# Kernel optimization log

Measured on AMD Instinct MI355X. Metric: run time of the kernel, lower is better.

Reference implementation:

```python
import jax, jax.numpy as jnp
import numpy as np

B, K, D, DK, DG, H = 4, 512, 768, 96, 96, 8  # batch, proposals, appearance, key, geo, n_relations


def setup_inputs() -> dict:
    key = jax.random.key(0)
    ks = jax.random.split(key, 12)
    s = 0.02
    return {
        "f_a": jax.random.normal(ks[0], (B, K, D), dtype=jnp.float32),
        "position_embedding": jax.random.uniform(ks[1], (B, K, K, DG), dtype=jnp.float32),
        "WG_w": jax.random.normal(ks[2], (H, DG), dtype=jnp.float32) * s,
        "WG_b": jnp.zeros((H,), dtype=jnp.float32),
        "WK_w": jax.random.normal(ks[3], (H, D, DK), dtype=jnp.float32) * s,
        "WK_b": jnp.zeros((H, DK), dtype=jnp.float32),
        "WQ_w": jax.random.normal(ks[4], (H, D, DK), dtype=jnp.float32) * s,
        "WQ_b": jnp.zeros((H, DK), dtype=jnp.float32),
        "WV_w": jax.random.normal(ks[5], (H, D, DK), dtype=jnp.float32) * s,
        "WV_b": jnp.zeros((H, DK), dtype=jnp.float32),
        "gamma": jnp.asarray(0.5, dtype=jnp.float32),
    }


def reference(f_a, position_embedding, WG_w, WG_b, WK_w, WK_b, WQ_w, WQ_b, WV_w, WV_b, gamma):
    dim_k = WK_w.shape[-1]
    # per-head projections: (B,K,D) x (H,D,DK) -> (B,H,K,DK)
    w_k = jnp.einsum('bkd,hdf->bhkf', f_a, WK_w) + WK_b[None, :, None, :]
    w_q = jnp.einsum('bkd,hdf->bhkf', f_a, WQ_w) + WQ_b[None, :, None, :]
    w_v = jnp.einsum('bkd,hdf->bhkf', f_a, WV_w) + WV_b[None, :, None, :]
    # scaled_dot[b,h,i,j] = <w_k[b,h,i], w_q[b,h,j]> / sqrt(dim_k)  (i: key row, j: query col)
    scores = jnp.einsum('bhif,bhjf->bhij', w_k, w_q) / np.sqrt(dim_k)
    # geometric gate: WG is Linear(DG, 1) per head, then ReLU -> (B,H,K,K)
    w_g = jax.nn.relu(jnp.einsum('bijg,hg->bhij', position_embedding, WG_w)
                      + WG_b[None, :, None, None])
    logits = jnp.log(jnp.clip(w_g, 1e-6, None)) + scores
    # torch Softmax(dim=1) over (B,K,K) = over the key index i -> axis 2 here
    attn = jax.nn.softmax(logits, axis=2)
    # output[b,j] = sum_i attn[b,h,i,j] * w_v[b,h,i,:]  -> (B,K,H,DK)
    out = jnp.einsum('bhij,bhif->bjhf', attn, w_v)
    b, k = f_a.shape[:2]
    concat = out.reshape(b, k, -1)  # concat over Nr heads, last dim = H*DK = D
    return gamma * concat + f_a
```

## Files before the change

kernel.cpp:

```cpp
#include <hip/hip_runtime.h>
#include <hip/hip_bf16.h>

#define B_ 4
#define K_ 512
#define D_ 768
#define DK_ 96
#define DG_ 96
#define H_ 8

typedef __attribute__((ext_vector_type(8))) __bf16 bf16x8;
typedef __attribute__((ext_vector_type(4))) float f32x4;

static __device__ __forceinline__ unsigned short f2bf(float x) {
  union { float f; unsigned int u; } v; v.f = x;
  unsigned int u = v.u;
  return (unsigned short)((u + 0x7FFFu + ((u >> 16) & 1u)) >> 16);
}
static __device__ __forceinline__ float bf2f(unsigned short u) {
  union { unsigned int u; float f; } v; v.u = ((unsigned int)u) << 16;
  return v.f;
}

__global__ __launch_bounds__(256) void prep_kernel(const float* __restrict__ fa,
                                                   unsigned short* __restrict__ fa16f,
                                                   const float* __restrict__ wq,
                                                   const float* __restrict__ wk,
                                                   const float* __restrict__ wv,
                                                   unsigned short* __restrict__ wt16f) {
  __shared__ unsigned short Ts[96][130];
  if (blockIdx.x < 768) {
    int idx = blockIdx.x * 256 + threadIdx.x;
    int row = idx / 96;
    int d0  = (idx % 96) * 8;
    int rowblk = row >> 4, lr = row & 15;
    int kk = d0 >> 5, lg = (d0 >> 3) & 3;
    const float4* src = (const float4*)(fa + (size_t)row * D_ + d0);
    float4 v0 = src[0], v1 = src[1];
    ushort4 o0, o1;
    o0.x = f2bf(v0.x); o0.y = f2bf(v0.y); o0.z = f2bf(v0.z); o0.w = f2bf(v0.w);
    o1.x = f2bf(v1.x); o1.y = f2bf(v1.y); o1.z = f2bf(v1.z); o1.w = f2bf(v1.w);
    unsigned short* dst = fa16f + (((size_t)rowblk * 24 + kk) * 64 + lg * 16 + lr) * 8;
    ((ushort4*)dst)[0] = o0;
    ((ushort4*)dst)[1] = o1;
  } else {
    int bid = blockIdx.x - 768;
    int dt = bid % 6; int rest = bid / 6;
    int h = rest % 8; int p = rest / 8;
    int ph = p * 8 + h;
    const float* w = (p == 0) ? wq : (p == 1) ? wk : wv;
    const float* src = w + ((size_t)h * D_ + dt * 128) * DK_;
    for (int c = threadIdx.x; c < 128 * 96; c += 256) {
      int dd = c / 96, f = c % 96;
      Ts[f][dd] = f2bf(src[c]);
    }
    __syncthreads();
    for (int c = threadIdx.x; c < 96 * 32; c += 256) {
      int f = c / 32, q = c % 32;
      int kk = dt * 4 + (q >> 3);
      int lg = (q >> 1) & 3;
      int e  = (q & 1) * 4;
      ushort4 v;
      v.x = Ts[f][q * 4 + 0]; v.y = Ts[f][q * 4 + 1];
      v.z = Ts[f][q * 4 + 2]; v.w = Ts[f][q * 4 + 3];
      unsigned short* dst = wt16f +
          ((((size_t)ph * 6 + (f >> 4)) * 24 + kk) * 64 + lg * 16 + (f & 15)) * 8 + e;
      *(ushort4*)dst = v;
    }
  }
}

__global__ __launch_bounds__(256) void proj_kernel(
    const unsigned short* __restrict__ fa16f, const unsigned short* __restrict__ wt16f,
    const float* __restrict__ bq, const float* __restrict__ bk, const float* __restrict__ bv,
    unsigned short* __restrict__ q16, unsigned short* __restrict__ k16,
    unsigned short* __restrict__ vt16) {
  __shared__ unsigned short Ts[96][130];
  int bid = blockIdx.x;
  int xcd = bid & 7, loc = bid >> 3;
  int b = xcd >> 1, half = xcd & 1;
  int ph = half * 12 + (loc >> 2);
  int mt = loc & 3;
  int p = ph >> 3, h = ph & 7;
  int lane = threadIdx.x & 63, wid = threadIdx.x >> 6;
  int lr = lane & 15, lg = lane >> 4;
  int row0 = mt * 128 + wid * 32;
  int rb0 = b * 32 + mt * 8 + wid * 2;

  const unsigned short* A  = fa16f + ((size_t)rb0 * 24) * 512 + lane * 8;
  const unsigned short* Bt = wt16f + ((size_t)ph * 6 * 24) * 512 + lane * 8;

  f32x4 acc[2][6];
#pragma unroll
  for (int i = 0; i < 2; i++)
#pragma unroll
    for (int c = 0; c < 6; c++) acc[i][c] = (f32x4){0.f, 0.f, 0.f, 0.f};

  auto LOADF = [&](bf16x8& a0, bf16x8& a1, bf16x8 (&bb)[6], int kk) {
    a0 = *(const bf16x8*)(A + (size_t)kk * 512);
    a1 = *(const bf16x8*)(A + ((size_t)24 + kk) * 512);
#pragma unroll
    for (int c = 0; c < 6; c++)
      bb[c] = *(const bf16x8*)(Bt + ((size_t)c * 24 + kk) * 512);
  };
  auto MF = [&](bf16x8& a0, bf16x8& a1, bf16x8 (&bb)[6]) {
#pragma unroll
    for (int c = 0; c < 6; c++) {
      acc[0][c] = __builtin_amdgcn_mfma_f32_16x16x32_bf16(a0, bb[c], acc[0][c], 0, 0, 0);
      acc[1][c] = __builtin_amdgcn_mfma_f32_16x16x32_bf16(a1, bb[c], acc[1][c], 0, 0, 0);
    }
  };

  bf16x8 a0X, a1X, bX[6], a0Y, a1Y, bY[6];
  LOADF(a0X, a1X, bX, 0);
  for (int kk = 0; kk < 24; kk += 2) {
    LOADF(a0Y, a1Y, bY, kk + 1);
    MF(a0X, a1X, bX);
    if (kk + 2 < 24) LOADF(a0X, a1X, bX, kk + 2);
    MF(a0Y, a1Y, bY);
  }

  const float* bias = (p == 0) ? bq : (p == 1) ? bk : bv;
  if (p == 2) {
#pragma unroll
    for (int i = 0; i < 2; i++)
#pragma unroll
      for (int c = 0; c < 6; c++) {
        int col = c * 16 + lr;
        float bb = bias[h * DK_ + col];
#pragma unroll
        for (int r = 0; r < 4; r++) {
          int lrow = wid * 32 + i * 16 + lg * 4 + r;
          Ts[col][lrow] = f2bf(acc[i][c][r] + bb);
        }
      }
    __syncthreads();
    unsigned short* dst = vt16 + (size_t)(b * H_ + h) * DK_ * K_ + mt * 128;
    for (int c2 = threadIdx.x; c2 < 96 * 32; c2 += 256) {
      int f = c2 / 32, q = c2 % 32;
      ushort4 v;
      v.x = Ts[f][q * 4 + 0]; v.y = Ts[f][q * 4 + 1];
      v.z = Ts[f][q * 4 + 2]; v.w = Ts[f][q * 4 + 3];
      *(ushort4*)(dst + (size_t)f * K_ + q * 4) = v;
    }
  } else {
    unsigned short* dst = (p == 0) ? q16 : k16;
#pragma unroll
    for (int i = 0; i < 2; i++)
#pragma unroll
      for (int c = 0; c < 6; c++) {
        int col = c * 16 + lr;
        float bb = bias[h * DK_ + col];
#pragma unroll
        for (int r = 0; r < 4; r++) {
          int row = row0 + i * 16 + lg * 4 + r;
          dst[((size_t)(b * H_ + h) * K_ + row) * DK_ + col] = f2bf(acc[i][c][r] + bb);
        }
      }
  }
}

__global__ __launch_bounds__(256) void scores_kernel(const unsigned short* __restrict__ q16,
                                                     const unsigned short* __restrict__ k16,
                                                     unsigned short* __restrict__ L16) {
  int bid = blockIdx.x;
  int xcd = bid & 7, loc = bid >> 3;
  int bh = ((loc >> 4) << 3) | xcd;
  int jt = (loc >> 2) & 3, it = loc & 3;
  int b = bh >> 3, h = bh & 7;
  int lane = threadIdx.x & 63, wid = threadIdx.x >> 6;
  int lr = lane & 15, lg = lane >> 4;
  int j0 = jt * 128 + wid * 32;
  int i0 = it * 128;
  const unsigned short* Q  = q16 + ((size_t)(b * H_ + h) * K_ + j0) * DK_;
  const unsigned short* Kp = k16 + ((size_t)(b * H_ + h) * K_ + i0) * DK_;

  f32x4 acc[2][8];
#pragma unroll
  for (int x = 0; x < 2; x++)
#pragma unroll
    for (int c = 0; c < 8; c++) acc[x][c] = (f32x4){0.f, 0.f, 0.f, 0.f};

#pragma unroll
  for (int kk = 0; kk < 3; kk++) {
    bf16x8 a0 = *(const bf16x8*)(Q + (size_t)lr * DK_ + kk * 32 + lg * 8);
    bf16x8 a1 = *(const bf16x8*)(Q + (size_t)(16 + lr) * DK_ + kk * 32 + lg * 8);
#pragma unroll
    for (int c = 0; c < 8; c++) {
      bf16x8 bfr = *(const bf16x8*)(Kp + (size_t)(c * 16 + lr) * DK_ + kk * 32 + lg * 8);
      acc[0][c] = __builtin_amdgcn_mfma_f32_16x16x32_bf16(a0, bfr, acc[0][c], 0, 0, 0);
      acc[1][c] = __builtin_amdgcn_mfma_f32_16x16x32_bf16(a1, bfr, acc[1][c], 0, 0, 0);
    }
  }

  const float scale = 0.10206207261596577f;
  unsigned short* Lb = L16 + ((size_t)(b * H_ + h) * K_ + j0) * K_ + i0;
#pragma unroll
  for (int x = 0; x < 2; x++)
#pragma unroll
    for (int c = 0; c < 8; c++)
#pragma unroll
      for (int r = 0; r < 4; r++) {
        int jl = x * 16 + lg * 4 + r;
        int il = c * 16 + lr;
        Lb[(size_t)jl * K_ + il] = f2bf(acc[x][c][r] * scale);
      }
}

#define GS_PAD 516
__global__ __launch_bounds__(512) void gatesm_kernel(
    const float* __restrict__ pe, const float* __restrict__ wgw,
    const float* __restrict__ wgb, const unsigned short* __restrict__ L16,
    unsigned short* __restrict__ p16) {
  extern __shared__ float Ls[];
  int b = blockIdx.x >> 7;
  int j0 = (blockIdx.x & 127) * 4;
  int t = threadIdx.x;
  int wv = t >> 6, lane = t & 63;
  int lr3 = (lane >> 3) & 7;
  int lg3 = lane & 7;
  const float4* pe4 = (const float4*)pe;
  const float4* wg4 = (const float4*)wgw;

  for (int p = 0; p < 8; p++) {
    int i = wv * 64 + p * 8 + lr3;
    float4 pev[4][3];
#pragma unroll
    for (int j = 0; j < 4; j++) {
      size_t base = ((size_t)(b * K_ + i) * K_ + (j0 + j)) * (DG_ / 4);
#pragma unroll
      for (int c = 0; c < 3; c++) pev[j][c] = pe4[base + lg3 + 8 * c];
    }
#pragma unroll
    for (int h = 0; h < H_; h++) {
      float4 w0 = wg4[h * 24 + lg3];
      float4 w1 = wg4[h * 24 + lg3 + 8];
      float4 w2 = wg4[h * 24 + lg3 + 16];
      float bias = wgb[h];
      float acc[4];
#pragma unroll
      for (int j = 0; j < 4; j++) {
        acc[j] = pev[j][0].x * w0.x + pev[j][0].y * w0.y + pev[j][0].z * w0.z + pev[j][0].w * w0.w
               + pev[j][1].x * w1.x + pev[j][1].y * w1.y + pev[j][1].z * w1.z + pev[j][1].w * w1.w
               + pev[j][2].x * w2.x + pev[j][2].y * w2.y + pev[j][2].z * w2.z + pev[j][2].w * w2.w;
      }
#pragma unroll
      for (int j = 0; j < 4; j++) {
        acc[j] += __shfl_xor(acc[j], 1);
        acc[j] += __shfl_xor(acc[j], 2);
        acc[j] += __shfl_xor(acc[j], 4);
      }
      if (lg3 == h) {
#pragma unroll
        for (int j = 0; j < 4; j++) {
          float lgt = __logf(fmaxf(acc[j] + bias, 1e-6f));
          Ls[(h * 4 + j) * GS_PAD + i] = lgt;
        }
      }
    }
  }
  __syncthreads();

#pragma unroll
  for (int rr = 0; rr < 4; rr++) {
    int row = wv * 4 + rr;
    int h = row >> 2, j = row & 3;
    const float* Lr = &Ls[row * GS_PAD];
    const unsigned short* Lg = L16 + ((size_t)(b * H_ + h) * K_ + (j0 + j)) * K_;
    float4 g0 = *(const float4*)(Lr + lane * 4);
    float4 g1 = *(const float4*)(Lr + 256 + lane * 4);
    ushort4 s0 = *(const ushort4*)(Lg + lane * 4);
    ushort4 s1 = *(const ushort4*)(Lg + 256 + lane * 4);
    float l0 = g0.x + bf2f(s0.x), l1 = g0.y + bf2f(s0.y);
    float l2 = g0.z + bf2f(s0.z), l3 = g0.w + bf2f(s0.w);
    float l4 = g1.x + bf2f(s1.x), l5 = g1.y + bf2f(s1.y);
    float l6 = g1.z + bf2f(s1.z), l7 = g1.w + bf2f(s1.w);
    float m = fmaxf(fmaxf(fmaxf(l0, l1), fmaxf(l2, l3)),
                    fmaxf(fmaxf(l4, l5), fmaxf(l6, l7)));
#pragma unroll
    for (int o = 32; o > 0; o >>= 1) m = fmaxf(m, __shfl_xor(m, o));
    float e0 = __expf(l0 - m), e1 = __expf(l1 - m), e2 = __expf(l2 - m), e3 = __expf(l3 - m);
    float e4 = __expf(l4 - m), e5 = __expf(l5 - m), e6 = __expf(l6 - m), e7 = __expf(l7 - m);
    float s = ((e0 + e1) + (e2 + e3)) + ((e4 + e5) + (e6 + e7));
#pragma unroll
    for (int o = 32; o > 0; o >>= 1) s += __shfl_xor(s, o);
    float inv = 1.0f / s;
    ushort4 o0, o1;
    o0.x = f2bf(e0 * inv); o0.y = f2bf(e1 * inv); o0.z = f2bf(e2 * inv); o0.w = f2bf(e3 * inv);
    o1.x = f2bf(e4 * inv); o1.y = f2bf(e5 * inv); o1.z = f2bf(e6 * inv); o1.w = f2bf(e7 * inv);
    ushort4* dst = (ushort4*)(p16 + ((size_t)(b * H_ + h) * K_ + (j0 + j)) * K_);
    dst[lane] = o0;
    dst[lane + 64] = o1;
  }
}

__global__ __launch_bounds__(256) void pv_kernel(const unsigned short* __restrict__ p16,
                                                 const unsigned short* __restrict__ vt16,
                                                 const float* __restrict__ fa,
                                                 const float* __restrict__ gptr,
                                                 float* __restrict__ out) {
  int bid = blockIdx.x;
  int xcd = bid & 7, loc = bid >> 3;
  int bh = ((loc >> 3) << 3) | xcd;
  int mt = loc & 7;
  int b = bh >> 3, h = bh & 7;
  int lane = threadIdx.x & 63, wid = threadIdx.x >> 6;
  int lr = lane & 15, lg = lane >> 4;
  int row0 = mt * 64 + wid * 16;
  const unsigned short* A = p16 + ((size_t)bh * K_ + row0) * K_;
  const unsigned short* V = vt16 + (size_t)bh * DK_ * K_;

  f32x4 acc[6];
#pragma unroll
  for (int c = 0; c < 6; c++) acc[c] = (f32x4){0.f, 0.f, 0.f, 0.f};

  for (int kk = 0; kk < 16; kk++) {
    bf16x8 a = *(const bf16x8*)(A + (size_t)lr * K_ + kk * 32 + lg * 8);
#pragma unroll
    for (int c = 0; c < 6; c++) {
      bf16x8 bfr = *(const bf16x8*)(V + (size_t)(c * 16 + lr) * K_ + kk * 32 + lg * 8);
      acc[c] = __builtin_amdgcn_mfma_f32_16x16x32_bf16(a, bfr, acc[c], 0, 0, 0);
    }
  }

  float gamma = gptr[0];
#pragma unroll
  for (int c = 0; c < 6; c++) {
    int fcol = c * 16 + lr;
#pragma unroll
    for (int r = 0; r < 4; r++) {
      int j = row0 + lg * 4 + r;
      size_t oidx = ((size_t)(b * K_ + j)) * D_ + h * DK_ + fcol;
      out[oidx] = gamma * acc[c][r] + fa[oidx];
    }
  }
}

extern "C" void kernel_launch(void* const* d_in, const int* in_sizes, int n_in,
                              void* d_out, int out_size, void* d_ws, size_t ws_size,
                              hipStream_t stream) {
  (void)in_sizes; (void)n_in; (void)out_size; (void)ws_size;
  const float* fa   = (const float*)d_in[0];
  const float* pe   = (const float*)d_in[1];
  const float* wgw  = (const float*)d_in[2];
  const float* wgb  = (const float*)d_in[3];
  const float* wkw  = (const float*)d_in[4];
  const float* wkb  = (const float*)d_in[5];
  const float* wqw  = (const float*)d_in[6];
  const float* wqb  = (const float*)d_in[7];
  const float* wvw  = (const float*)d_in[8];
  const float* wvb  = (const float*)d_in[9];
  const float* gptr = (const float*)d_in[10];
  float* out = (float*)d_out;

  char* ws = (char*)d_ws;
  unsigned short* fa16f = (unsigned short*)ws; ws += (size_t)B_ * K_ * D_ * 2;
  unsigned short* wt16f = (unsigned short*)ws; ws += (size_t)3 * H_ * DK_ * D_ * 2;
  unsigned short* q16   = (unsigned short*)ws; ws += (size_t)B_ * H_ * K_ * DK_ * 2;
  unsigned short* k16   = (unsigned short*)ws; ws += (size_t)B_ * H_ * K_ * DK_ * 2;
  unsigned short* vt16  = (unsigned short*)ws; ws += (size_t)B_ * H_ * DK_ * K_ * 2;
  unsigned short* L16   = (unsigned short*)ws; ws += (size_t)B_ * H_ * K_ * K_ * 2;
  unsigned short* p16   = (unsigned short*)ws;

  const int lds_bytes = 32 * GS_PAD * 4;
  hipFuncSetAttribute((const void*)gatesm_kernel,
                      hipFuncAttributeMaxDynamicSharedMemorySize, lds_bytes);

  prep_kernel<<<768 + 144, 256, 0, stream>>>(fa, fa16f, wqw, wkw, wvw, wt16f);
  proj_kernel<<<384, 256, 0, stream>>>(fa16f, wt16f, wqb, wkb, wvb, q16, k16, vt16);
  scores_kernel<<<512, 256, 0, stream>>>(q16, k16, L16);
  gatesm_kernel<<<B_ * 128, 512, lds_bytes, stream>>>(pe, wgw, wgb, L16, p16);
  pv_kernel<<<256, 256, 0, stream>>>(p16, vt16, fa, gptr, out);
}
```

Measured before the change: 160.1 us.

## Store Q, K and V^T in MFMA fragment-swizzled layout for coalesced loads

The projection kernel now writes Q, K and transposed V in a pre-swizzled fragment layout, so each lane's 8-element bf16 operand sits contiguously at lane*8. The scores and PV kernels then read their MFMA operands as fully coalesced 512-element blocks instead of row-strided gathers. This is meant to cut memory transactions and cache-line waste in the scores and PV operand loads. In exchange, the Q and K stores in the projection kernel become scattered 2-byte writes, and the V transpose uses a different LDS read pattern with a padded 132-wide tile.

```diff
diff --git a/kernel.cpp b/kernel.cpp
--- a/kernel.cpp
+++ b/kernel.cpp
@@ -72,9 +72,9 @@
 __global__ __launch_bounds__(256) void proj_kernel(
     const unsigned short* __restrict__ fa16f, const unsigned short* __restrict__ wt16f,
     const float* __restrict__ bq, const float* __restrict__ bk, const float* __restrict__ bv,
-    unsigned short* __restrict__ q16, unsigned short* __restrict__ k16,
-    unsigned short* __restrict__ vt16) {
-  __shared__ unsigned short Ts[96][130];
+    unsigned short* __restrict__ q16f, unsigned short* __restrict__ k16f,
+    unsigned short* __restrict__ vt16f) {
+  __shared__ unsigned short Ts[96][132];
   int bid = blockIdx.x;
   int xcd = bid & 7, loc = bid >> 3;
   int b = xcd >> 1, half = xcd & 1;
@@ -83,7 +83,6 @@
   int p = ph >> 3, h = ph & 7;
   int lane = threadIdx.x & 63, wid = threadIdx.x >> 6;
   int lr = lane & 15, lg = lane >> 4;
-  int row0 = mt * 128 + wid * 32;
   int rb0 = b * 32 + mt * 8 + wid * 2;
 
   const unsigned short* A  = fa16f + ((size_t)rb0 * 24) * 512 + lane * 8;
@@ -134,33 +133,42 @@
         }
       }
     __syncthreads();
-    unsigned short* dst = vt16 + (size_t)(b * H_ + h) * DK_ * K_ + mt * 128;
-    for (int c2 = threadIdx.x; c2 < 96 * 32; c2 += 256) {
-      int f = c2 / 32, q = c2 % 32;
-      ushort4 v;
-      v.x = Ts[f][q * 4 + 0]; v.y = Ts[f][q * 4 + 1];
-      v.z = Ts[f][q * 4 + 2]; v.w = Ts[f][q * 4 + 3];
-      *(ushort4*)(dst + (size_t)f * K_ + q * 4) = v;
+    unsigned short* dst = vt16f + (size_t)(b * H_ + h) * 49152;
+    for (int c2 = threadIdx.x; c2 < 1536; c2 += 256) {
+      int lane_d = c2 & 63;
+      int kkl = (c2 >> 6) & 3;
+      int fblk = c2 >> 8;
+      int f = fblk * 16 + (lane_d & 15);
+      int il = kkl * 32 + (lane_d >> 4) * 8;
+      ushort4 v0 = *(const ushort4*)&Ts[f][il];
+      ushort4 v1 = *(const ushort4*)&Ts[f][il + 4];
+      unsigned short* o = dst + (((size_t)fblk * 16 + (mt * 4 + kkl)) * 64 + lane_d) * 8;
+      ((ushort4*)o)[0] = v0;
+      ((ushort4*)o)[1] = v1;
     }
   } else {
-    unsigned short* dst = (p == 0) ? q16 : k16;
-#pragma unroll
-    for (int i = 0; i < 2; i++)
+    unsigned short* dst = ((p == 0) ? q16f : k16f) + (size_t)(b * H_ + h) * 49152;
+#pragma unroll
+    for (int i = 0; i < 2; i++) {
+      int rowblk = mt * 8 + wid * 2 + i;
 #pragma unroll
       for (int c = 0; c < 6; c++) {
         int col = c * 16 + lr;
+        int kk = col >> 5, klg = (col >> 3) & 3, e = col & 7;
         float bb = bias[h * DK_ + col];
 #pragma unroll
         for (int r = 0; r < 4; r++) {
-          int row = row0 + i * 16 + lg * 4 + r;
-          dst[((size_t)(b * H_ + h) * K_ + row) * DK_ + col] = f2bf(acc[i][c][r] + bb);
+          int row_lr = lg * 4 + r;
+          dst[(((size_t)rowblk * 3 + kk) * 64 + klg * 16 + row_lr) * 8 + e] =
+              f2bf(acc[i][c][r] + bb);
         }
       }
-  }
-}
-
-__global__ __launch_bounds__(256) void scores_kernel(const unsigned short* __restrict__ q16,
-                                                     const unsigned short* __restrict__ k16,
+    }
+  }
+}
+
+__global__ __launch_bounds__(256) void scores_kernel(const unsigned short* __restrict__ q16f,
+                                                     const unsigned short* __restrict__ k16f,
                                                      unsigned short* __restrict__ L16) {
   int bid = blockIdx.x;
   int xcd = bid & 7, loc = bid >> 3;
@@ -171,8 +179,9 @@
   int lr = lane & 15, lg = lane >> 4;
   int j0 = jt * 128 + wid * 32;
   int i0 = it * 128;
-  const unsigned short* Q  = q16 + ((size_t)(b * H_ + h) * K_ + j0) * DK_;
-  const unsigned short* Kp = k16 + ((size_t)(b * H_ + h) * K_ + i0) * DK_;
+  const unsigned short* Qf = q16f + (size_t)bh * 49152 + lane * 8;
+  const unsigned short* Kf = k16f + (size_t)bh * 49152 + lane * 8;
+  int jb0 = jt * 8 + wid * 2;
 
   f32x4 acc[2][8];
 #pragma unroll
@@ -182,18 +191,18 @@
 
 #pragma unroll
   for (int kk = 0; kk < 3; kk++) {
-    bf16x8 a0 = *(const bf16x8*)(Q + (size_t)lr * DK_ + kk * 32 + lg * 8);
-    bf16x8 a1 = *(const bf16x8*)(Q + (size_t)(16 + lr) * DK_ + kk * 32 + lg * 8);
+    bf16x8 a0 = *(const bf16x8*)(Qf + ((size_t)(jb0 + 0) * 3 + kk) * 512);
+    bf16x8 a1 = *(const bf16x8*)(Qf + ((size_t)(jb0 + 1) * 3 + kk) * 512);
 #pragma unroll
     for (int c = 0; c < 8; c++) {
-      bf16x8 bfr = *(const bf16x8*)(Kp + (size_t)(c * 16 + lr) * DK_ + kk * 32 + lg * 8);
+      bf16x8 bfr = *(const bf16x8*)(Kf + ((size_t)(it * 8 + c) * 3 + kk) * 512);
       acc[0][c] = __builtin_amdgcn_mfma_f32_16x16x32_bf16(a0, bfr, acc[0][c], 0, 0, 0);
       acc[1][c] = __builtin_amdgcn_mfma_f32_16x16x32_bf16(a1, bfr, acc[1][c], 0, 0, 0);
     }
   }
 
   const float scale = 0.10206207261596577f;
-  unsigned short* Lb = L16 + ((size_t)(b * H_ + h) * K_ + j0) * K_ + i0;
+  unsigned short* Lb = L16 + ((size_t)bh * K_ + j0) * K_ + i0;
 #pragma unroll
   for (int x = 0; x < 2; x++)
 #pragma unroll
@@ -294,7 +303,7 @@
 }
 
 __global__ __launch_bounds__(256) void pv_kernel(const unsigned short* __restrict__ p16,
-                                                 const unsigned short* __restrict__ vt16,
+                                                 const unsigned short* __restrict__ vt16f,
                                                  const float* __restrict__ fa,
                                                  const float* __restrict__ gptr,
                                                  float* __restrict__ out) {
@@ -306,8 +315,8 @@
   int lane = threadIdx.x & 63, wid = threadIdx.x >> 6;
   int lr = lane & 15, lg = lane >> 4;
   int row0 = mt * 64 + wid * 16;
-  const unsigned short* A = p16 + ((size_t)bh * K_ + row0) * K_;
-  const unsigned short* V = vt16 + (size_t)bh * DK_ * K_;
+  const unsigned short* A  = p16 + ((size_t)bh * K_ + row0) * K_;
+  const unsigned short* Vf = vt16f + (size_t)bh * 49152 + lane * 8;
 
   f32x4 acc[6];
 #pragma unroll
@@ -317,7 +326,7 @@
     bf16x8 a = *(const bf16x8*)(A + (size_t)lr * K_ + kk * 32 + lg * 8);
 #pragma unroll
     for (int c = 0; c < 6; c++) {
-      bf16x8 bfr = *(const bf16x8*)(V + (size_t)(c * 16 + lr) * K_ + kk * 32 + lg * 8);
+      bf16x8 bfr = *(const bf16x8*)(Vf + ((size_t)c * 16 + kk) * 512);
       acc[c] = __builtin_amdgcn_mfma_f32_16x16x32_bf16(a, bfr, acc[c], 0, 0, 0);
     }
   }
@@ -355,9 +364,9 @@
   char* ws = (char*)d_ws;
   unsigned short* fa16f = (unsigned short*)ws; ws += (size_t)B_ * K_ * D_ * 2;
   unsigned short* wt16f = (unsigned short*)ws; ws += (size_t)3 * H_ * DK_ * D_ * 2;
-  unsigned short* q16   = (unsigned short*)ws; ws += (size_t)B_ * H_ * K_ * DK_ * 2;
-  unsigned short* k16   = (unsigned short*)ws; ws += (size_t)B_ * H_ * K_ * DK_ * 2;
-  unsigned short* vt16  = (unsigned short*)ws; ws += (size_t)B_ * H_ * DK_ * K_ * 2;
+  unsigned short* q16f  = (unsigned short*)ws; ws += (size_t)B_ * H_ * K_ * DK_ * 2;
+  unsigned short* k16f  = (unsigned short*)ws; ws += (size_t)B_ * H_ * K_ * DK_ * 2;
+  unsigned short* vt16f = (unsigned short*)ws; ws += (size_t)B_ * H_ * DK_ * K_ * 2;
   unsigned short* L16   = (unsigned short*)ws; ws += (size_t)B_ * H_ * K_ * K_ * 2;
   unsigned short* p16   = (unsigned short*)ws;
 
@@ -366,8 +375,8 @@
                       hipFuncAttributeMaxDynamicSharedMemorySize, lds_bytes);
 
   prep_kernel<<<768 + 144, 256, 0, stream>>>(fa, fa16f, wqw, wkw, wvw, wt16f);
-  proj_kernel<<<384, 256, 0, stream>>>(fa16f, wt16f, wqb, wkb, wvb, q16, k16, vt16);
-  scores_kernel<<<512, 256, 0, stream>>>(q16, k16, L16);
+  proj_kernel<<<384, 256, 0, stream>>>(fa16f, wt16f, wqb, wkb, wvb, q16f, k16f, vt16f);
+  scores_kernel<<<512, 256, 0, stream>>>(q16f, k16f, L16);
   gatesm_kernel<<<B_ * 128, 512, lds_bytes, stream>>>(pe, wgw, wgb, L16, p16);
-  pv_kernel<<<256, 256, 0, stream>>>(p16, vt16, fa, gptr, out);
-}
+  pv_kernel<<<256, 256, 0, stream>>>(p16, vt16f, fa, gptr, out);
+}
```

After: 154.6 us. 1.04x faster.
